# Performance work log

Measured on AMD Instinct MI355X. Metric: run time of the kernel, lower is better.

The kernel has to match this reference:

```python
import jax, jax.numpy as jnp
import numpy as np


def _dwconv(x, w, pad):
    # depthwise conv, x: [B,C,H,W], w: [C,1,kh,kw]
    return jax.lax.conv_general_dilated(
        x, w, (1, 1), [(pad, pad), (pad, pad)],
        dimension_numbers=('NCHW', 'OIHW', 'NCHW'),
        feature_group_count=x.shape[1])


def _hw_to_wh(x, h, w):
    # rearrange 'b (h w) c -> b (w h) c'
    b, t, c = x.shape
    return x.reshape(b, h, w, c).transpose(0, 2, 1, 3).reshape(b, t, c)


def _wkv(decay, first, k, v):
    # Vision-RWKV WKV: decay/first [C4]; k, v [B, T, C4]
    w_neg = -jnp.exp(decay)  # RUN_CUDA applies w = -exp(w)
    u = first

    def step(carry, kv):
        p, q, o = carry
        kt, vt = kv
        no = jnp.maximum(o, u + kt)
        A = jnp.exp(o - no)
        Bx = jnp.exp(u + kt - no)
        y = (A * p + Bx * vt) / (A * q + Bx)
        no2 = jnp.maximum(o + w_neg, kt)
        A2 = jnp.exp(o + w_neg - no2)
        B2 = jnp.exp(kt - no2)
        return (A2 * p + B2 * vt, A2 * q + B2, no2), y

    Bn, T, C4 = k.shape
    init = (jnp.zeros((Bn, C4), k.dtype), jnp.zeros((Bn, C4), k.dtype),
            jnp.full((Bn, C4), -1e38, k.dtype))
    _, ys = jax.lax.scan(step, init, (jnp.swapaxes(k, 0, 1), jnp.swapaxes(v, 0, 1)))
    return jnp.swapaxes(ys, 0, 1)  # [B, T, C4]


def setup_inputs() -> dict:
    key = jax.random.key(0)
    ks = jax.random.split(key, 16)
    B, H, W, C = 8, 64, 64, 256
    T = H * W
    C4 = 4 * C
    s = 1.0 / np.sqrt(C)
    return {
        'x': jax.random.normal(ks[0], (B, T, C), jnp.float32),
        'alpha': jax.random.normal(ks[1], (4,), jnp.float32) * 0.5,
        'dw1': jax.random.normal(ks[2], (C, 1, 1, 1), jnp.float32) * s,
        'dw3': jax.random.normal(ks[3], (C, 1, 3, 3), jnp.float32) * s,
        'dw5': jax.random.normal(ks[4], (C, 1, 5, 5), jnp.float32) * s,
        'Wk': jax.random.normal(ks[5], (C, C), jnp.float32) * s,
        'Wv': jax.random.normal(ks[6], (C, C), jnp.float32) * s,
        'Wr': jax.random.normal(ks[7], (C, C), jnp.float32) * s,
        'Wf': jax.random.normal(ks[8], (C, C), jnp.float32) * s,
        'bf': jax.random.normal(ks[9], (C,), jnp.float32) * 0.02,
        'Wb': jax.random.normal(ks[10], (C, C), jnp.float32) * s,
        'bb': jax.random.normal(ks[11], (C,), jnp.float32) * 0.02,
        'spatial_decay': jax.random.normal(ks[12], (C4,), jnp.float32),
        'spatial_first': jax.random.normal(ks[13], (C4,), jnp.float32),
        'Wo': jax.random.normal(ks[14], (C, C4), jnp.float32) * (1.0 / np.sqrt(C4)),
        'h': H,
        'w': W,
    }


def reference(x, alpha, dw1, dw3, dw5, Wk, Wv, Wr, Wf, bf, Wb, bb,
              spatial_decay, spatial_first, Wo, h, w):
    B, T, C = x.shape
    # OmniShift (training path): alpha-weighted identity + depthwise 1/3/5 convs
    xi = x.reshape(B, h, w, C).transpose(0, 3, 1, 2)  # [B,C,H,W]
    xsft = (alpha[0] * xi + alpha[1] * _dwconv(xi, dw1, 0)
            + alpha[2] * _dwconv(xi, dw3, 1) + alpha[3] * _dwconv(xi, dw5, 2))
    xf = xsft.transpose(0, 2, 3, 1).reshape(B, T, C)  # [B,T,C]
    k = xf @ Wk.T
    v = xf @ Wv.T
    sr = jax.nn.sigmoid(xf @ Wr.T)
    # 1x1 conv1d over channels == linear with bias
    k1 = k @ Wf.T + bf
    v1 = v @ Wf.T + bf
    k3 = k @ Wb.T + bb
    v3 = v @ Wb.T + bb
    k2 = _hw_to_wh(k1, h, w)
    v2 = _hw_to_wh(v1, h, w)
    k4 = _hw_to_wh(k3, h, w)
    v4 = _hw_to_wh(v3, h, w)
    ks_ = jnp.concatenate([k1, k2, k3, k4], axis=2)  # [B,T,4C]
    vs_ = jnp.concatenate([v1, v2, v3, v4], axis=2)
    srs = jnp.concatenate([sr, sr, sr, sr], axis=2)
    Tf = jnp.asarray(T, x.dtype)
    xs = _wkv(spatial_decay / Tf, spatial_first / Tf, ks_, vs_)
    return (xs * srs) @ Wo.T  # [B,T,C]
```

## Files before the change

kernel.cpp:

```cpp
#include <hip/hip_runtime.h>

typedef __attribute__((ext_vector_type(8))) short bf16x8;
typedef __attribute__((ext_vector_type(4))) float f32x4;
typedef __attribute__((ext_vector_type(4))) unsigned short u16x4;
typedef __attribute__((ext_vector_type(2))) unsigned short u16x2;
typedef __attribute__((ext_vector_type(8))) unsigned short u16x8;

#define GLD16(g, l) __builtin_amdgcn_global_load_lds( \
    (const __attribute__((address_space(1))) void*)(g), \
    (__attribute__((address_space(3))) void*)(l), 16, 0, 0)

__device__ __forceinline__ unsigned short f2bf(float f) {
  unsigned u = __float_as_uint(f);
  unsigned r = u + 0x7FFFu + ((u >> 16) & 1u);
  return (unsigned short)(r >> 16);
}
__device__ __forceinline__ float bf2f(unsigned short h) {
  return __uint_as_float(((unsigned)h) << 16);
}


__global__ void k_weff(const float* __restrict__ alpha,
                       const float* __restrict__ dw1,
                       const float* __restrict__ dw3,
                       const float* __restrict__ dw5,
                       float* __restrict__ weff) {
  int tap = blockIdx.x;
  int c = threadIdx.x;
  int dy = tap / 5, dx = tap % 5;
  float v = alpha[3] * dw5[c * 25 + tap];
  if (dy >= 1 && dy <= 3 && dx >= 1 && dx <= 3)
    v += alpha[2] * dw3[c * 9 + (dy - 1) * 3 + (dx - 1)];
  if (tap == 12) v += alpha[1] * dw1[c] + alpha[0];
  weff[tap * 256 + c] = v;
}

__global__ void k_combine(const float* __restrict__ Wk,
                          const float* __restrict__ Wv,
                          const float* __restrict__ Wr,
                          const float* __restrict__ Wf,
                          const float* __restrict__ Wb,
                          const float* __restrict__ bfv,
                          const float* __restrict__ bbv,
                          short* __restrict__ wcat,
                          float* __restrict__ bias) {
  int mat = blockIdx.x >> 8;
  int i = blockIdx.x & 255;
  int j = threadIdx.x;
  if (mat == 4) {
    wcat[(size_t)(1024 + i) * 256 + j] = (short)f2bf(Wr[i * 256 + j]);
    if (j == 0) bias[1024 + i] = 0.f;
    return;
  }
  const float* Am = (mat & 1) ? Wb : Wf;
  const float* Bm = (mat < 2) ? Wk : Wv;
  const float* arow = Am + i * 256;
  float acc = 0.f;
  for (int m = 0; m < 256; ++m) acc += arow[m] * Bm[m * 256 + j];
  int newrow = ((mat & 1) << 9) + (i << 1) + (mat >> 1);
  wcat[(size_t)newrow * 256 + j] = (short)f2bf(acc);
  if (j == 0) bias[newrow] = (mat & 1) ? bbv[i] : bfv[i];
}

__global__ void k_wo(const float* __restrict__ Wo, short* __restrict__ wob) {
  int i = blockIdx.x * 256 + threadIdx.x;
  wob[i] = (short)f2bf(Wo[i]);
}

__global__ __launch_bounds__(256, 8)
void k_shift(const float* __restrict__ x, const float* __restrict__ weff,
             unsigned short* __restrict__ xf) {
  int c = threadIdx.x;
  int w0 = blockIdx.x * 8;
  int h0 = blockIdx.y * 2;
  int b = blockIdx.z;

  float wg[5][5];
#pragma unroll
  for (int dy = 0; dy < 5; ++dy)
#pragma unroll
    for (int dx = 0; dx < 5; ++dx)
      wg[dy][dx] = weff[(dy * 5 + dx) * 256 + c];

  const float* xb = x + (size_t)b * 4096 * 256 + c;
  int rowoff[6];
  bool rv[6];
#pragma unroll
  for (int r = 0; r < 6; ++r) {
    int y = h0 + r - 2;
    rv[r] = (y >= 0 && y < 64);
    int yc = y < 0 ? 0 : (y > 63 ? 63 : y);
    rowoff[r] = yc * 64 * 256;
  }

  float win[6][8];
#pragma unroll
  for (int j = -2; j <= 1; ++j) {
    int xx = w0 + j;
    int slot = j & 7;
    bool xv = (xx >= 0);
    int xc = xx < 0 ? 0 : xx;
#pragma unroll
    for (int r = 0; r < 6; ++r) {
      float v = xb[rowoff[r] + xc * 256];
      win[r][slot] = (xv && rv[r]) ? v : 0.f;
    }
  }

  unsigned short* xo = xf + ((size_t)b * 4096 + (size_t)h0 * 64) * 256 + c;
#pragma unroll
  for (int ui = 0; ui < 8; ++ui) {
    int w = w0 + ui;
    {
      int xx = w + 2;
      int slot = (ui + 2) & 7;
      bool xv = (xx < 64);
      int xc = xx > 63 ? 63 : xx;
#pragma unroll
      for (int r = 0; r < 6; ++r) {
        float v = xb[rowoff[r] + xc * 256];
        win[r][slot] = (xv && rv[r]) ? v : 0.f;
      }
    }
#pragma unroll
    for (int j = 0; j < 2; ++j) {
      float a0 = 0.f, a1 = 0.f, a2 = 0.f, a3 = 0.f, a4 = 0.f;
#pragma unroll
      for (int dx = 0; dx < 5; ++dx) {
        int slot = (ui - 2 + dx) & 7;
        a0 = fmaf(win[j + 0][slot], wg[0][dx], a0);
        a1 = fmaf(win[j + 1][slot], wg[1][dx], a1);
        a2 = fmaf(win[j + 2][slot], wg[2][dx], a2);
        a3 = fmaf(win[j + 3][slot], wg[3][dx], a3);
        a4 = fmaf(win[j + 4][slot], wg[4][dx], a4);
      }
      xo[((size_t)j * 64 + w) * 256] = f2bf(((a0 + a1) + (a2 + a3)) + a4);
    }
  }
}

template <int EPI, int BM, int BK, int SWZ>
__global__ __launch_bounds__(256, (BK == 128) ? 3 : 4)
void gemm_bt(const short* __restrict__ A, const short* __restrict__ Bm,
             const float* __restrict__ bias,
             void* __restrict__ O0, void* __restrict__ O1,
             int M, int N, int K) {
  constexpr int AE = BM * BK;
  constexpr int MI = BM / 32;
  constexpr int CH = BK / 8;
  constexpr int LA = BM * BK / 2048;
  constexpr int LB = BK / 16;
  constexpr int RW = 132;
  __shared__ __align__(16) short lds[AE + 128 * BK];

  int t = threadIdx.x;
  int lane = t & 63, wv = t >> 6;
  int wr = wv >> 1, wc = wv & 1;
  int m0, n0;
  if (SWZ) {
    int x = blockIdx.x & 7;
    int j = blockIdx.x >> 3;
    m0 = (x * 32 + j / 10) * BM;
    n0 = (j % 10) * 128;
  } else {
    m0 = blockIdx.x * BM;
    n0 = blockIdx.y * 128;
  }
  f32x4 acc[MI][4] = {};

  for (int k0 = 0; k0 < K; k0 += BK) {
#pragma unroll
    for (int i = 0; i < LA; ++i) {
      int cc = t + i * 256;
      int row = cc / CH, kc = cc % CH;
      GLD16(A + (size_t)(m0 + row) * K + k0 + ((kc ^ (row & (CH - 1))) << 3), &lds[cc * 8]);
    }
#pragma unroll
    for (int i = 0; i < LB; ++i) {
      int cc = t + i * 256;
      int row = cc / CH, kc = cc % CH;
      GLD16(Bm + (size_t)(n0 + row) * K + k0 + ((kc ^ (row & (CH - 1))) << 3), &lds[AE + cc * 8]);
    }
    __syncthreads();
#pragma unroll
    for (int kk = 0; kk < BK / 32; ++kk) {
      int ch = kk * 4 + (lane >> 4);
      bf16x8 av[MI], bv[4];
#pragma unroll
      for (int i = 0; i < MI; ++i) {
        int row = wr * (BM / 2) + i * 16 + (lane & 15);
        av[i] = *(const bf16x8*)&lds[row * BK + ((ch ^ (row & (CH - 1))) << 3)];
      }
#pragma unroll
      for (int i = 0; i < 4; ++i) {
        int row = wc * 64 + i * 16 + (lane & 15);
        bv[i] = *(const bf16x8*)&lds[AE + row * BK + ((ch ^ (row & (CH - 1))) << 3)];
      }
#pragma unroll
      for (int mi = 0; mi < MI; ++mi)
#pragma unroll
        for (int ni = 0; ni < 4; ++ni)
          acc[mi][ni] = __builtin_amdgcn_mfma_f32_16x16x32_bf16(av[mi], bv[ni], acc[mi][ni], 0, 0, 0);
    }
    __syncthreads();
  }

  float* fl = (float*)lds;
  float bb[4];
  if (EPI == 0) {
#pragma unroll
    for (int ni = 0; ni < 4; ++ni)
      bb[ni] = bias[n0 + wc * 64 + ni * 16 + (lane & 15)];
  }
  int rrow = t >> 3;
  int colb = (t & 7) * 16;
#pragma unroll
  for (int mi = 0; mi < MI; ++mi) {
    if (mi) __syncthreads();
    {
      int r0 = (lane >> 4) * 4;
#pragma unroll
      for (int ni = 0; ni < 4; ++ni) {
        int colL = wc * 64 + (lane & 15) + ni * 16;
        f32x4 v = acc[mi][ni];
#pragma unroll
        for (int j = 0; j < 4; ++j) {
          float vj = v[j];
          if (EPI == 0) vj += bb[ni];
          fl[(wr * 16 + r0 + j) * RW + colL] = vj;
        }
      }
    }
    __syncthreads();
    float vv[16];
#pragma unroll
    for (int q = 0; q < 4; ++q)
      *(f32x4*)&vv[q * 4] = *(const f32x4*)&fl[rrow * RW + colb + q * 4];
    int grow = m0 + (rrow >> 4) * (BM / 2) + mi * 16 + (rrow & 15);
    if (EPI == 0) {
      u16x8 o0, o1;
      if (n0 < 1024) {
#pragma unroll
        for (int q = 0; q < 8; ++q) { o0[q] = f2bf(vv[q]); o1[q] = f2bf(vv[8 + q]); }
        unsigned short* dst = (unsigned short*)O0 + (size_t)grow * 1024 + n0 + colb;
        *(u16x8*)dst = o0;
        *(u16x8*)(dst + 8) = o1;
      } else {
#pragma unroll
        for (int q = 0; q < 8; ++q) {
          o0[q] = f2bf(1.f / (1.f + __expf(-vv[q])));
          o1[q] = f2bf(1.f / (1.f + __expf(-vv[8 + q])));
        }
        unsigned short* dst = (unsigned short*)O1 + (size_t)grow * 256 + (n0 - 1024) + colb;
        *(u16x8*)dst = o0;
        *(u16x8*)(dst + 8) = o1;
      }
    } else {
      float* dst = (float*)O0 + (size_t)grow * N + n0 + colb;
#pragma unroll
      for (int q = 0; q < 4; ++q) {
        f32x4 ov = {vv[q * 4], vv[q * 4 + 1], vv[q * 4 + 2], vv[q * 4 + 3]};
        *(f32x4*)(dst + q * 4) = ov;
      }
    }
  }
}

__global__ __launch_bounds__(256, 8)
void k_wkv(const unsigned short* __restrict__ kvb, const unsigned short* __restrict__ srb,
           const float* __restrict__ decay, const float* __restrict__ first,
           unsigned short* __restrict__ xssr) {
  const int T = 4096;
  int tid = threadIdx.x;
  int g = tid >> 7;
  int l = tid & 127;
  int c0 = l * 2;
  int tr = blockIdx.y;
  int s = (g << 1) | tr;
  int scol = s * 256;
  int chunk = blockIdx.x;
  int b = blockIdx.z;
  const float invT = 1.0f / 4096.0f;

  float P0 = 0.f, P1 = 0.f, Q0 = 0.f, Q1 = 0.f;
  float D0 = __expf(-__expf(decay[scol + c0] * invT));
  float D1 = __expf(-__expf(decay[scol + c0 + 1] * invT));
  float eu0 = __expf(first[scol + c0] * invT);
  float eu1 = __expf(first[scol + c0 + 1] * invT);

  int t0 = chunk * 32;
  int tstart = t0 >= 16 ? t0 - 16 : 0;
  int tend = t0 + 32;
  const size_t bT = (size_t)b * T;
  const int kvoff = (g << 9) + (c0 << 1);

  auto kvload = [&](int tt) {
    int tok = tr ? (((tt & 63) << 6) | (tt >> 6)) : tt;
    return *(const u16x4*)(kvb + (bT + tok) * 1024 + kvoff);
  };
  auto srload = [&](int tt) {
    return *(const u16x2*)(srb + (bT + tt) * 256 + c0);
  };

  u16x4 kvA = kvload(tstart);
  u16x4 kvB = kvload(tstart + 1);
  u16x2 svA = srload(tstart);
  u16x2 svB = srload(tstart + 1);

  for (int tt = tstart; tt < tend; tt += 2) {
    int tp2 = tt + 2 < tend ? tt + 2 : tend - 1;
    int tp3 = tt + 3 < tend ? tt + 3 : tend - 1;
    u16x4 kvC = kvload(tp2);
    u16x4 kvD = kvload(tp3);
    u16x2 svC = srload(tp2);
    u16x2 svD = srload(tp3);

#pragma unroll
    for (int u = 0; u < 2; ++u) {
      int ti = tt + u;
      u16x4 kv4 = u ? kvB : kvA;
      u16x2 sv = u ? svB : svA;
      float k0 = bf2f(kv4[0]), v0 = bf2f(kv4[1]);
      float k1 = bf2f(kv4[2]), v1 = bf2f(kv4[3]);
      float e0 = __expf(k0), e1 = __expf(k1);
      if (ti >= t0) {
        float t0e = e0 * eu0, t1e = e1 * eu1;
        float y0 = fmaf(t0e, v0, P0) * __builtin_amdgcn_rcpf(Q0 + t0e);
        float y1 = fmaf(t1e, v1, P1) * __builtin_amdgcn_rcpf(Q1 + t1e);
        u16x2 ow;
        ow[0] = f2bf(y0 * bf2f(sv[0]));
        ow[1] = f2bf(y1 * bf2f(sv[1]));
        *(u16x2*)(xssr + (bT + ti) * 1024 + scol + c0) = ow;
      }
      P0 = fmaf(P0, D0, e0 * v0);
      Q0 = fmaf(Q0, D0, e0);
      P1 = fmaf(P1, D1, e1 * v1);
      Q1 = fmaf(Q1, D1, e1);
    }
    kvA = kvC; kvB = kvD;
    svA = svC; svB = svD;
  }
}

extern "C" void kernel_launch(void* const* d_in, const int* in_sizes, int n_in,
                              void* d_out, int out_size, void* d_ws, size_t ws_size,
                              hipStream_t stream) {
  const float* x      = (const float*)d_in[0];
  const float* alpha  = (const float*)d_in[1];
  const float* dw1    = (const float*)d_in[2];
  const float* dw3    = (const float*)d_in[3];
  const float* dw5    = (const float*)d_in[4];
  const float* Wk     = (const float*)d_in[5];
  const float* Wv     = (const float*)d_in[6];
  const float* Wr     = (const float*)d_in[7];
  const float* Wf     = (const float*)d_in[8];
  const float* bfv    = (const float*)d_in[9];
  const float* Wb     = (const float*)d_in[10];
  const float* bbv    = (const float*)d_in[11];
  const float* sdecay = (const float*)d_in[12];
  const float* sfirst = (const float*)d_in[13];
  const float* Wo     = (const float*)d_in[14];
  (void)n_in; (void)out_size; (void)ws_size;

  const int Bn = in_sizes[0] / (4096 * 256);
  const int MT = Bn * 4096;

  char* ws = (char*)d_ws;
  size_t off = 0;
  auto alloc = [&](size_t bytes) {
    void* p = ws + off;
    off += (bytes + 255) & ~(size_t)255;
    return p;
  };
  short* xf            = (short*)alloc((size_t)MT * 256 * 2);
  unsigned short* kv   = (unsigned short*)alloc((size_t)MT * 1024 * 2);
  unsigned short* srb  = (unsigned short*)alloc((size_t)MT * 256 * 2);
  unsigned short* xssr = (unsigned short*)alloc((size_t)MT * 1024 * 2);
  short* wcat          = (short*)alloc((size_t)1280 * 256 * 2);
  float* bias          = (float*)alloc(1280 * 4);
  float* weff          = (float*)alloc(25 * 256 * 4);
  short* wob           = (short*)alloc((size_t)256 * 1024 * 2);

  k_weff<<<25, 256, 0, stream>>>(alpha, dw1, dw3, dw5, weff);
  k_combine<<<1280, 256, 0, stream>>>(Wk, Wv, Wr, Wf, Wb, bfv, bbv, wcat, bias);
  k_wo<<<1024, 256, 0, stream>>>(Wo, wob);
  k_shift<<<dim3(8, 32, Bn), 256, 0, stream>>>(x, weff, (unsigned short*)xf);
  gemm_bt<0, 128, 64, 1><<<dim3(MT / 128 * 10), 256, 0, stream>>>(
      xf, wcat, bias, kv, srb, MT, 1280, 256);
  k_wkv<<<dim3(128, 2, Bn), 256, 0, stream>>>(kv, srb, sdecay, sfirst, xssr);
  gemm_bt<1, 64, 128, 0><<<dim3(MT / 64, 2), 256, 0, stream>>>(
      (const short*)xssr, wob, nullptr, d_out, nullptr, MT, 256, 1024);
}
```

Before: 165.7 us.

## Double-buffer GEMM LDS tiles with async global-to-LDS prefetch two steps ahead

Replaces the single-buffered GEMM main loop with a two-buffer pipeline. The next k-tiles are issued via global_load_lds while the current tile is computed, and readiness is tracked with explicit vmcnt waits and raw barriers. The second GEMM's BK drops from 128 to 64 so the doubled LDS fits, and launch-bound occupancy hints are lowered. The aim is to hide global load latency, at the cost of more LDS per block and lower occupancy. The hand-written vmcnt waits are tied to the per-stage load count LD, so correctness depends on that count matching the number of loads issued.

```diff
diff --git a/kernel.cpp b/kernel.cpp
--- a/kernel.cpp
+++ b/kernel.cpp
@@ -17,6 +17,14 @@
 }
 __device__ __forceinline__ float bf2f(unsigned short h) {
   return __uint_as_float(((unsigned)h) << 16);
+}
+
+template <int N>
+__device__ __forceinline__ void wait_vm() {
+  if constexpr (N == 0) asm volatile("s_waitcnt vmcnt(0)" ::: "memory");
+  else if constexpr (N == 6) asm volatile("s_waitcnt vmcnt(6)" ::: "memory");
+  else if constexpr (N == 8) asm volatile("s_waitcnt vmcnt(8)" ::: "memory");
+  else static_assert(N == 0, "unsupported vmcnt");
 }
 
 
@@ -140,18 +148,20 @@
 }
 
 template <int EPI, int BM, int BK, int SWZ>
-__global__ __launch_bounds__(256, (BK == 128) ? 3 : 4)
-void gemm_bt(const short* __restrict__ A, const short* __restrict__ Bm,
+__global__ __launch_bounds__(256, (BM == 128) ? 2 : 3)
+void gemm_db(const short* __restrict__ A, const short* __restrict__ Bm,
              const float* __restrict__ bias,
              void* __restrict__ O0, void* __restrict__ O1,
              int M, int N, int K) {
   constexpr int AE = BM * BK;
+  constexpr int BUFS = (BM + 128) * BK;
   constexpr int MI = BM / 32;
   constexpr int CH = BK / 8;
   constexpr int LA = BM * BK / 2048;
   constexpr int LB = BK / 16;
+  constexpr int LD = LA + LB;
   constexpr int RW = 132;
-  __shared__ __align__(16) short lds[AE + 128 * BK];
+  __shared__ __align__(16) short lds[2 * BUFS];
 
   int t = threadIdx.x;
   int lane = t & 63, wv = t >> 6;
@@ -166,22 +176,34 @@
     m0 = blockIdx.x * BM;
     n0 = blockIdx.y * 128;
   }
+  const int NK = K / BK;
   f32x4 acc[MI][4] = {};
 
-  for (int k0 = 0; k0 < K; k0 += BK) {
+  float bb[4];
+  if (EPI == 0) {
+#pragma unroll
+    for (int ni = 0; ni < 4; ++ni)
+      bb[ni] = bias[n0 + wc * 64 + ni * 16 + (lane & 15)];
+  }
+
+  auto STAGE = [&](int step, int bo) {
+    int k0 = step * BK;
 #pragma unroll
     for (int i = 0; i < LA; ++i) {
       int cc = t + i * 256;
       int row = cc / CH, kc = cc % CH;
-      GLD16(A + (size_t)(m0 + row) * K + k0 + ((kc ^ (row & (CH - 1))) << 3), &lds[cc * 8]);
+      GLD16(A + (size_t)(m0 + row) * K + k0 + ((kc ^ (row & (CH - 1))) << 3),
+            &lds[bo + cc * 8]);
     }
 #pragma unroll
     for (int i = 0; i < LB; ++i) {
       int cc = t + i * 256;
       int row = cc / CH, kc = cc % CH;
-      GLD16(Bm + (size_t)(n0 + row) * K + k0 + ((kc ^ (row & (CH - 1))) << 3), &lds[AE + cc * 8]);
-    }
-    __syncthreads();
+      GLD16(Bm + (size_t)(n0 + row) * K + k0 + ((kc ^ (row & (CH - 1))) << 3),
+            &lds[bo + AE + cc * 8]);
+    }
+  };
+  auto COMPUTE = [&](int bo) {
 #pragma unroll
     for (int kk = 0; kk < BK / 32; ++kk) {
       int ch = kk * 4 + (lane >> 4);
@@ -189,12 +211,12 @@
 #pragma unroll
       for (int i = 0; i < MI; ++i) {
         int row = wr * (BM / 2) + i * 16 + (lane & 15);
-        av[i] = *(const bf16x8*)&lds[row * BK + ((ch ^ (row & (CH - 1))) << 3)];
+        av[i] = *(const bf16x8*)&lds[bo + row * BK + ((ch ^ (row & (CH - 1))) << 3)];
       }
 #pragma unroll
       for (int i = 0; i < 4; ++i) {
         int row = wc * 64 + i * 16 + (lane & 15);
-        bv[i] = *(const bf16x8*)&lds[AE + row * BK + ((ch ^ (row & (CH - 1))) << 3)];
+        bv[i] = *(const bf16x8*)&lds[bo + AE + row * BK + ((ch ^ (row & (CH - 1))) << 3)];
       }
 #pragma unroll
       for (int mi = 0; mi < MI; ++mi)
@@ -202,16 +224,24 @@
         for (int ni = 0; ni < 4; ++ni)
           acc[mi][ni] = __builtin_amdgcn_mfma_f32_16x16x32_bf16(av[mi], bv[ni], acc[mi][ni], 0, 0, 0);
     }
-    __syncthreads();
+  };
+
+  STAGE(0, 0);
+  STAGE(1, BUFS);
+#pragma unroll
+  for (int k = 0; k < 16; ++k) {
+    if (k >= NK) break;
+    int bo = (k & 1) ? BUFS : 0;
+    if (k < NK - 1) wait_vm<LD>();
+    else wait_vm<0>();
+    __builtin_amdgcn_s_barrier();
+    COMPUTE(bo);
+    asm volatile("s_waitcnt lgkmcnt(0)" ::: "memory");
+    __builtin_amdgcn_s_barrier();
+    if (k + 2 < NK) STAGE(k + 2, bo);
   }
 
   float* fl = (float*)lds;
-  float bb[4];
-  if (EPI == 0) {
-#pragma unroll
-    for (int ni = 0; ni < 4; ++ni)
-      bb[ni] = bias[n0 + wc * 64 + ni * 16 + (lane & 15)];
-  }
   int rrow = t >> 3;
   int colb = (t & 7) * 16;
 #pragma unroll
@@ -385,9 +415,9 @@
   k_combine<<<1280, 256, 0, stream>>>(Wk, Wv, Wr, Wf, Wb, bfv, bbv, wcat, bias);
   k_wo<<<1024, 256, 0, stream>>>(Wo, wob);
   k_shift<<<dim3(8, 32, Bn), 256, 0, stream>>>(x, weff, (unsigned short*)xf);
-  gemm_bt<0, 128, 64, 1><<<dim3(MT / 128 * 10), 256, 0, stream>>>(
+  gemm_db<0, 128, 64, 1><<<dim3(MT / 128 * 10), 256, 0, stream>>>(
       xf, wcat, bias, kv, srb, MT, 1280, 256);
   k_wkv<<<dim3(128, 2, Bn), 256, 0, stream>>>(kv, srb, sdecay, sfirst, xssr);
-  gemm_bt<1, 64, 128, 0><<<dim3(MT / 64, 2), 256, 0, stream>>>(
+  gemm_db<1, 64, 64, 0><<<dim3(MT / 64, 2), 256, 0, stream>>>(
       (const short*)xssr, wob, nullptr, d_out, nullptr, MT, 256, 1024);
 }
```

Measured after the change: 165.9 us. About the same (+0.1%).
